# Kernel tuning notes

Hardware: AMD Instinct MI355X
Metric: run time of the kernel (lower is better)

## Reference

```python
import jax, jax.numpy as jnp
import numpy as np

TEMP = 0.5  # init kwarg `tmp`
NUM_CLASSES = 100


def setup_inputs() -> dict:
    key = jax.random.key(0)
    k1, k2 = jax.random.split(key)
    embedding = jax.random.normal(k1, (8192, 256), dtype=jnp.float32)
    label = jax.random.randint(k2, (8192,), 0, NUM_CLASSES, dtype=jnp.int64)
    return {"embedding": embedding, "label": label}


def reference(embedding, label):
    # Row-normalize -> pairwise cosine similarity [N, N]
    normed = embedding / jnp.linalg.norm(embedding, axis=1, keepdims=True)
    sim = (normed @ normed.T) / TEMP  # already divided by temperature

    N = embedding.shape[0]
    eye = jnp.eye(N, dtype=bool)

    # Denominator: sum of exp(sim) over off-diagonal entries per row
    exp_sim = jnp.exp(sim)
    row_sum = jnp.sum(jnp.where(eye, 0.0, exp_sim), axis=1)  # [N]

    # log(exp(sim_ij) / row_sum_i) = sim_ij - log(row_sum_i)
    log_prob = sim - jnp.log(row_sum)[:, None]

    # Positive mask: same label, i != j
    pos_mask = (label[:, None] == label[None, :]) & ~eye
    n_i = jnp.sum(pos_mask, axis=1)  # positives per anchor

    inner = jnp.sum(jnp.where(pos_mask, log_prob, 0.0), axis=1)  # [N]
    per_anchor = jnp.where(n_i > 0, -inner / jnp.maximum(n_i, 1).astype(sim.dtype), 0.0)
    return jnp.sum(per_anchor)
```

## Files before the change

### kernel.cpp

```cpp
#include <hip/hip_runtime.h>
#include <hip/hip_bf16.h>
#include <stdint.h>

#define N    8192
#define D    256
#define NCLS 100

static constexpr float TEMP    = 0.5f;
static constexpr float SCALE_F = 1.69864360f;
static constexpr float LN2     = 0.69314718055994531f;

typedef float f32x4 __attribute__((ext_vector_type(4)));

__device__ __forceinline__ unsigned short f2bf(float f) {
  union { float f; unsigned int u; } x; x.f = f;
  unsigned int r = x.u + 0x7fffu + ((x.u >> 16) & 1u);
  return (unsigned short)(r >> 16);
}
__device__ __forceinline__ float bf2f(unsigned short b) {
  union { unsigned int u; float f; } x; x.u = ((unsigned int)b) << 16;
  return x.f;
}
__device__ __forceinline__ void gld16(const void* g, void* l) {
  __builtin_amdgcn_global_load_lds(
      (const __attribute__((address_space(1))) unsigned int*)g,
      (__attribute__((address_space(3))) unsigned int*)l, 16, 0, 0);
}


__global__ __launch_bounds__(256) void normalize_kernel(
    const float* __restrict__ emb, const long long* __restrict__ label,
    unsigned short* __restrict__ abf, unsigned char* __restrict__ a8,
    float* __restrict__ rowsum, int* __restrict__ cnt,
    int* __restrict__ list) {
  const int row  = blockIdx.x * 4 + (threadIdx.x >> 6);
  const int lane = threadIdx.x & 63;
  const float4 v = ((const float4*)(emb + (size_t)row * D))[lane];
  float ss = v.x * v.x + v.y * v.y + v.z * v.z + v.w * v.w;
#pragma unroll
  for (int off = 1; off < 64; off <<= 1) ss += __shfl_xor(ss, off);
  const float s = rsqrtf(ss) * SCALE_F;
  const float x = v.x * s, y = v.y * s, z = v.z * s, wv = v.w * s;

  ushort4 o;
  o.x = f2bf(x); o.y = f2bf(y); o.z = f2bf(z); o.w = f2bf(wv);
  ((ushort4*)(abf + (size_t)row * D))[lane] = o;

  int p = __builtin_amdgcn_cvt_pk_fp8_f32(x, y, 0, false);
  p = __builtin_amdgcn_cvt_pk_fp8_f32(z, wv, p, true);
  *(int*)(a8 + (size_t)(row >> 4) * 4096 + (lane >> 1) * 128 +
          (row & 15) * 8 + (lane & 1) * 4) = p;

  if (lane == 0) {
    rowsum[row] = 0.f;
    const int c = (int)label[row];
    const int slot = atomicAdd(cnt + c, 1);
    list[c * 256 + slot] = row;
  }
}

#define TM 128
#define TN 128
#define JT 4

__global__ __launch_bounds__(256, 3) void simexp_rowsum_kernel(
    const unsigned char* __restrict__ A, float* __restrict__ rowsum) {
  __shared__ __align__(16) unsigned char sa[TM * 256];
  __shared__ __align__(16) unsigned char sb[2][TN * 64];
  const int tid  = threadIdx.x;
  const int w    = tid >> 6;
  const int lane = tid & 63;
  const int quad = lane >> 4;
  const int l15  = lane & 15;
  const int row0 = blockIdx.y * TM;
  const int jc0  = blockIdx.x * (TN * JT);
  if (row0 >= jc0 + TN * JT) return;
  const int sdiag = (row0 >= jc0) ? ((row0 - jc0) >> 7) : -1;
  const int jt0   = (sdiag >= 0) ? sdiag : 0;
  const int pr0 = row0 >> 4;
  const int pam = (w & 1) * 4;
  const int pbn = (w >> 1) * 4;
  const int wm  = (w & 1) * 64;
  const int jn0 = (w >> 1) * 64;

#pragma unroll
  for (int p = 0; p < 8; ++p) {
    const int seg = w * 8 + p;
    gld16(A + (size_t)(pr0 + (seg >> 2)) * 4096 + (seg & 3) * 1024 + lane * 16,
          sa + seg * 1024);
  }
  {
    const int pj0 = (jc0 + jt0 * TN) >> 4;
#pragma unroll
    for (int p = 0; p < 2; ++p) {
      const int seg = w * 2 + p;
      gld16(A + (size_t)(pj0 + seg) * 4096 + lane * 16, sb[0] + seg * 1024);
    }
  }
  __syncthreads();

  float rowpart[4][4];
#pragma unroll
  for (int mt = 0; mt < 4; ++mt)
#pragma unroll
    for (int e = 0; e < 4; ++e) rowpart[mt][e] = 0.f;

  int buf = 0;
  for (int jt = jt0; jt < JT; ++jt) {
    f32x4 acc[4][4];
#pragma unroll
    for (int mt = 0; mt < 4; ++mt)
#pragma unroll
      for (int nt = 0; nt < 4; ++nt) acc[mt][nt] = (f32x4){0.f, 0.f, 0.f, 0.f};

#pragma unroll
    for (int kq = 0; kq < 4; ++kq) {
      if (!(jt == JT - 1 && kq == 3)) {
        const int njt = (kq == 3) ? jt + 1 : jt;
        const int nkq = (kq + 1) & 3;
        const int pj0 = (jc0 + njt * TN) >> 4;
#pragma unroll
        for (int p = 0; p < 2; ++p) {
          const int seg = w * 2 + p;
          gld16(A + (size_t)(pj0 + seg) * 4096 + nkq * 1024 + lane * 16,
                sb[buf ^ 1] + seg * 1024);
        }
      }
#pragma unroll
      for (int kkl = 0; kkl < 2; ++kkl) {
        const int fo = (kkl * 4 + quad) * 128 + l15 * 8;
        long af[4], bf[4];
#pragma unroll
        for (int mt = 0; mt < 4; ++mt)
          af[mt] = *(const long*)(sa + (pam + mt) * 4096 + kq * 1024 + fo);
#pragma unroll
        for (int nt = 0; nt < 4; ++nt)
          bf[nt] = *(const long*)(sb[buf] + (pbn + nt) * 1024 + fo);
#pragma unroll
        for (int mt = 0; mt < 4; ++mt)
#pragma unroll
          for (int nt = 0; nt < 4; ++nt)
            acc[mt][nt] = __builtin_amdgcn_mfma_f32_16x16x32_fp8_fp8(
                af[mt], bf[nt], acc[mt][nt], 0, 0, 0);
      }
      __syncthreads();
      buf ^= 1;
    }

    const bool diag = (jt == sdiag);
    float colpart[4] = {0.f, 0.f, 0.f, 0.f};
#pragma unroll
    for (int mt = 0; mt < 4; ++mt)
#pragma unroll
      for (int nt = 0; nt < 4; ++nt)
#pragma unroll
        for (int e = 0; e < 4; ++e) {
          float v = __builtin_amdgcn_exp2f(acc[mt][nt][e]);
          if (diag) {
            const int iloc = wm + mt * 16 + quad * 4 + e;
            const int jloc = jn0 + nt * 16 + l15;
            v = (iloc < jloc) ? v : 0.f;
          }
          rowpart[mt][e] += v;
          colpart[nt] += v;
        }
#pragma unroll
    for (int nt = 0; nt < 4; ++nt) {
      float v = colpart[nt];
      v += __shfl_xor(v, 16);
      v += __shfl_xor(v, 32);
      if (quad == 0)
        atomicAdd(&rowsum[jc0 + jt * TN + jn0 + nt * 16 + l15], v);
    }
  }

#pragma unroll
  for (int mt = 0; mt < 4; ++mt)
#pragma unroll
    for (int e = 0; e < 4; ++e) {
      float v = rowpart[mt][e];
      v += __shfl_xor(v, 1);
      v += __shfl_xor(v, 2);
      v += __shfl_xor(v, 4);
      v += __shfl_xor(v, 8);
      if (l15 == 0)
        atomicAdd(&rowsum[row0 + wm + mt * 16 + quad * 4 + e], v);
    }
}

__global__ __launch_bounds__(256) void finalize_kernel(
    const unsigned short* __restrict__ abf, const float* __restrict__ rowsum,
    const long long* __restrict__ label, const int* __restrict__ cnt,
    const int* __restrict__ list, float* __restrict__ out) {
  __shared__ float red[4];
  __shared__ int rows_l[256];
  const int tid  = threadIdx.x;
  const int w    = tid >> 6;
  const int lane = tid & 63;

  if (blockIdx.x < NCLS) {
    const int c = blockIdx.x;
    const int m = cnt[c];
    if (m <= 1) return;
    if (tid < m) rows_l[tid] = list[c * 256 + tid];
    __syncthreads();
    float acc = 0.f;
    for (int s = 0; s < m; ++s)
      acc += bf2f(abf[(size_t)rows_l[s] * D + tid]);
    float v = acc * acc;
#pragma unroll
    for (int off = 1; off < 64; off <<= 1) v += __shfl_xor(v, off);
    if (lane == 0) red[w] = v;
    __syncthreads();
    if (tid == 0) {
      const float ssq = red[0] + red[1] + red[2] + red[3];
      const float term = (ssq * LN2 - 2.0f * (float)m) / (float)(m - 1);
      atomicAdd(out, -term);
    }
  } else {
    const int i = (blockIdx.x - NCLS) * 256 + tid;
    const int c = (int)label[i];
    float v = 0.f;
    if (cnt[c] > 1)
      v = __builtin_amdgcn_logf(rowsum[i]) * LN2;
#pragma unroll
    for (int off = 1; off < 64; off <<= 1) v += __shfl_xor(v, off);
    if (lane == 0) red[w] = v;
    __syncthreads();
    if (tid == 0)
      atomicAdd(out, red[0] + red[1] + red[2] + red[3]);
  }
}

extern "C" void kernel_launch(void* const* d_in, const int* in_sizes, int n_in,
                              void* d_out, int out_size, void* d_ws,
                              size_t ws_size, hipStream_t stream) {
  const float* emb = (const float*)d_in[0];
  const long long* label = (const long long*)d_in[1];
  float* out = (float*)d_out;

  char* ws = (char*)d_ws;
  unsigned short* abf = (unsigned short*)ws;
  unsigned char* a8 = (unsigned char*)(ws + (size_t)N * D * 2);
  float* rowsum = (float*)(ws + (size_t)N * D * 3);
  int* cnt = (int*)(rowsum + N);
  int* list = cnt + 128;

  hipMemsetAsync(cnt, 0, 128 * 4, stream);
  hipMemsetAsync(out, 0, sizeof(float), stream);

  normalize_kernel<<<N / 4, 256, 0, stream>>>(emb, label, abf, a8, rowsum,
                                              cnt, list);

  dim3 gridB(N / (TN * JT), N / TM);
  simexp_rowsum_kernel<<<gridB, 256, 0, stream>>>(a8, rowsum);

  finalize_kernel<<<NCLS + N / 256, 256, 0, stream>>>(abf, rowsum, label, cnt,
                                                      list, out);
}
```

Before: 135.3 us.

## Load B fragments directly from global and launch only lower-triangle tiles

```diff
diff --git a/kernel.cpp b/kernel.cpp
--- a/kernel.cpp
+++ b/kernel.cpp
@@ -66,16 +66,21 @@
 __global__ __launch_bounds__(256, 3) void simexp_rowsum_kernel(
     const unsigned char* __restrict__ A, float* __restrict__ rowsum) {
   __shared__ __align__(16) unsigned char sa[TM * 256];
-  __shared__ __align__(16) unsigned char sb[2][TN * 64];
   const int tid  = threadIdx.x;
   const int w    = tid >> 6;
   const int lane = tid & 63;
   const int quad = lane >> 4;
   const int l15  = lane & 15;
-  const int row0 = blockIdx.y * TM;
-  const int jc0  = blockIdx.x * (TN * JT);
-  if (row0 >= jc0 + TN * JT) return;
-  const int sdiag = (row0 >= jc0) ? ((row0 - jc0) >> 7) : -1;
+
+  const int b = blockIdx.x;
+  int x = (int)((-1.0f + sqrtf(1.0f + 2.0f * (float)b)) * 0.5f);
+  while (2 * (x + 1) * (x + 1) + 2 * (x + 1) <= b) ++x;
+  while (2 * x * x + 2 * x > b) --x;
+  const int y = b - (2 * x * x + 2 * x);
+
+  const int row0 = y * TM;
+  const int jc0  = x * (TN * JT);
+  const int sdiag = (y >= 4 * x) ? (y - 4 * x) : -1;
   const int jt0   = (sdiag >= 0) ? sdiag : 0;
   const int pr0 = row0 >> 4;
   const int pam = (w & 1) * 4;
@@ -89,14 +94,6 @@
     gld16(A + (size_t)(pr0 + (seg >> 2)) * 4096 + (seg & 3) * 1024 + lane * 16,
           sa + seg * 1024);
   }
-  {
-    const int pj0 = (jc0 + jt0 * TN) >> 4;
-#pragma unroll
-    for (int p = 0; p < 2; ++p) {
-      const int seg = w * 2 + p;
-      gld16(A + (size_t)(pj0 + seg) * 4096 + lane * 16, sb[0] + seg * 1024);
-    }
-  }
   __syncthreads();
 
   float rowpart[4][4];
@@ -105,8 +102,10 @@
 #pragma unroll
     for (int e = 0; e < 4; ++e) rowpart[mt][e] = 0.f;
 
-  int buf = 0;
   for (int jt = jt0; jt < JT; ++jt) {
+    const unsigned char* Bp =
+        A + (size_t)(((jc0 + jt * TN) >> 4) + pbn) * 4096;
+
     f32x4 acc[4][4];
 #pragma unroll
     for (int mt = 0; mt < 4; ++mt)
@@ -115,27 +114,16 @@
 
 #pragma unroll
     for (int kq = 0; kq < 4; ++kq) {
-      if (!(jt == JT - 1 && kq == 3)) {
-        const int njt = (kq == 3) ? jt + 1 : jt;
-        const int nkq = (kq + 1) & 3;
-        const int pj0 = (jc0 + njt * TN) >> 4;
-#pragma unroll
-        for (int p = 0; p < 2; ++p) {
-          const int seg = w * 2 + p;
-          gld16(A + (size_t)(pj0 + seg) * 4096 + nkq * 1024 + lane * 16,
-                sb[buf ^ 1] + seg * 1024);
-        }
-      }
 #pragma unroll
       for (int kkl = 0; kkl < 2; ++kkl) {
         const int fo = (kkl * 4 + quad) * 128 + l15 * 8;
         long af[4], bf[4];
 #pragma unroll
+        for (int nt = 0; nt < 4; ++nt)
+          bf[nt] = *(const long*)(Bp + nt * 4096 + kq * 1024 + fo);
+#pragma unroll
         for (int mt = 0; mt < 4; ++mt)
           af[mt] = *(const long*)(sa + (pam + mt) * 4096 + kq * 1024 + fo);
-#pragma unroll
-        for (int nt = 0; nt < 4; ++nt)
-          bf[nt] = *(const long*)(sb[buf] + (pbn + nt) * 1024 + fo);
 #pragma unroll
         for (int mt = 0; mt < 4; ++mt)
 #pragma unroll
@@ -143,8 +131,6 @@
             acc[mt][nt] = __builtin_amdgcn_mfma_f32_16x16x32_fp8_fp8(
                 af[mt], bf[nt], acc[mt][nt], 0, 0, 0);
       }
-      __syncthreads();
-      buf ^= 1;
     }
 
     const bool diag = (jt == sdiag);
@@ -252,8 +238,7 @@
   normalize_kernel<<<N / 4, 256, 0, stream>>>(emb, label, abf, a8, rowsum,
                                               cnt, list);
 
-  dim3 gridB(N / (TN * JT), N / TM);
-  simexp_rowsum_kernel<<<gridB, 256, 0, stream>>>(a8, rowsum);
+  simexp_rowsum_kernel<<<544, 256, 0, stream>>>(a8, rowsum);
 
   finalize_kernel<<<NCLS + N / 256, 256, 0, stream>>>(abf, rowsum, label, cnt,
                                                       list, out);
```

After: 129.9 us. 4.0% less time.
